# Optimization experiments

Hardware: AMD Instinct MI355X
Metric: run time of the kernel (lower is better)

The kernel has to match this reference:

```python
import jax, jax.numpy as jnp
import numpy as np

HEADS = 8
DIM_HEAD = 64
LN_EPS = 1e-5


def _layernorm(x, gamma, beta):
    mu = jnp.mean(x, axis=-1, keepdims=True)
    var = jnp.var(x, axis=-1, keepdims=True)
    return (x - mu) * jax.lax.rsqrt(var + LN_EPS) * gamma + beta


def setup_inputs() -> dict:
    key = jax.random.key(0)
    ks = jax.random.split(key, 5)
    B, N, D = 1, 16384, 512
    return {
        "x": jax.random.normal(ks[0], (B, N, D), dtype=jnp.float32),
        "ln_gamma": jnp.ones((D,), dtype=jnp.float32),
        "ln_beta": jnp.zeros((D,), dtype=jnp.float32),
        "w_qkv": jax.random.normal(ks[1], (D, 3 * D), dtype=jnp.float32) * (D ** -0.5),
        "agent": jax.random.normal(ks[2], (HEADS, 512, DIM_HEAD), dtype=jnp.float32) * (DIM_HEAD ** -0.5),
        "w_out": jax.random.normal(ks[3], (D, D), dtype=jnp.float32) * (D ** -0.5),
        "b_out": jnp.zeros((D,), dtype=jnp.float32),
    }


def reference(x, ln_gamma, ln_beta, w_qkv, agent, w_out, b_out):
    # TransLayer: x + Mask_Agent_Attention(LayerNorm(x))
    B, N, D = x.shape
    xn = _layernorm(x, ln_gamma, ln_beta)

    qkv = xn @ w_qkv                                   # [B, N, 3D]
    q, k, v = jnp.split(qkv, 3, axis=-1)
    # [B, H, N, d]
    q = q.reshape(B, N, HEADS, DIM_HEAD).transpose(0, 2, 1, 3)
    k = k.reshape(B, N, HEADS, DIM_HEAD).transpose(0, 2, 1, 3)
    v = v.reshape(B, N, HEADS, DIM_HEAD).transpose(0, 2, 1, 3)

    scale = DIM_HEAD ** -0.5  # tem=0 -> classical 1/sqrt(d) scaling

    # agents aggregate values: softmax over keys  [B, H, A, N]
    attn1 = jax.nn.softmax(jnp.einsum('had,bhnd->bhan', agent, k) * scale, axis=-1)
    agent_v = jnp.einsum('bhan,bhnd->bhad', attn1, v)  # [B, H, A, d]

    # queries attend to agents: softmax over agents  [B, H, N, A]
    attn2 = jax.nn.softmax(jnp.einsum('bhnd,had->bhna', q, agent) * scale, axis=-1)
    out = jnp.einsum('bhna,bhad->bhnd', attn2, agent_v)  # [B, H, N, d]

    out = out + v  # residual=True: value residual inside attention
    out = out.transpose(0, 2, 1, 3).reshape(B, N, D)
    out = out @ w_out + b_out
    return x + out
```

## Files before the change

kernel.cpp:

```cpp
#include <hip/hip_runtime.h>
#include <stdint.h>

typedef unsigned short u16;
typedef __attribute__((ext_vector_type(8))) short bf16x8;
typedef __attribute__((ext_vector_type(4))) float f32x4;

__device__ __forceinline__ float bf2f(u16 u){
  union { uint32_t i; float f; } v; v.i = ((uint32_t)u) << 16; return v.f;
}
__device__ __forceinline__ u16 f2bf(float f){
  union { float fl; uint32_t i; } v; v.fl = f;
  uint32_t r = v.i + 0x7FFFu + ((v.i >> 16) & 1u);
  return (u16)(r >> 16);
}
__device__ __forceinline__ uint32_t cvt_pk_bf16(float lo, float hi){
  uint32_t r;
  asm("v_cvt_pk_bf16_f32 %0, %1, %2" : "=v"(r) : "v"(lo), "v"(hi));
  return r;
}
__device__ __forceinline__ f32x4 mfma16(bf16x8 a, bf16x8 b, f32x4 c){
  return __builtin_amdgcn_mfma_f32_16x16x32_bf16(a, b, c, 0, 0, 0);
}
__device__ __forceinline__ void gload16(const u16* g, u16* l){
  __builtin_amdgcn_global_load_lds((const __attribute__((address_space(1))) void*)g,
                                   (__attribute__((address_space(3))) void*)l, 16, 0, 0);
}

__global__ __launch_bounds__(256) void k_conv_bf(const float* __restrict__ in, u16* __restrict__ out, int n, float scale){
  int i = (blockIdx.x * 256 + threadIdx.x) * 4;
  if (i >= n) return;
  float4 v = *(const float4*)(in + i);
  ushort4 o; o.x=f2bf(v.x*scale); o.y=f2bf(v.y*scale); o.z=f2bf(v.z*scale); o.w=f2bf(v.w*scale);
  *(ushort4*)(out + i) = o;
}

__global__ __launch_bounds__(256) void k_transp(const float* __restrict__ in, u16* __restrict__ out, int R, int C){
  __shared__ u16 tile[64][68];
  int c0 = blockIdx.x * 64, r0 = blockIdx.y * 64;
  int tr = threadIdx.x >> 4;
  int tc = (threadIdx.x & 15) * 4;
  for (int rr = 0; rr < 4; rr++){
    int r = rr * 16 + tr;
    float4 v = *(const float4*)(in + (size_t)(r0 + r) * C + c0 + tc);
    ushort4 o; o.x=f2bf(v.x); o.y=f2bf(v.y); o.z=f2bf(v.z); o.w=f2bf(v.w);
    *(ushort4*)&tile[r][tc] = o;
  }
  __syncthreads();
  for (int rr = 0; rr < 4; rr++){
    int oc = rr * 16 + tr;
    ushort4 o;
    o.x = tile[tc+0][oc]; o.y = tile[tc+1][oc]; o.z = tile[tc+2][oc]; o.w = tile[tc+3][oc];
    *(ushort4*)(out + (size_t)(c0 + oc) * R + r0 + tc) = o;
  }
}

__global__ __launch_bounds__(256) void k_transp_v(const u16* __restrict__ qkv, u16* __restrict__ vT){
  __shared__ u16 tile[64][68];
  int n0 = blockIdx.x * 64;
  int c0 = blockIdx.y * 64;
  int tr = threadIdx.x >> 4;
  int tc = (threadIdx.x & 15) * 4;
  for (int rr = 0; rr < 4; rr++){
    int r = rr * 16 + tr;
    ushort4 v = *(const ushort4*)(qkv + (size_t)(n0 + r) * 1536 + 1024 + c0 + tc);
    *(ushort4*)&tile[r][tc] = v;
  }
  __syncthreads();
  for (int rr = 0; rr < 4; rr++){
    int oc = rr * 16 + tr;
    ushort4 o;
    o.x = tile[tc+0][oc]; o.y = tile[tc+1][oc]; o.z = tile[tc+2][oc]; o.w = tile[tc+3][oc];
    *(ushort4*)(vT + (size_t)(c0 + oc) * 16384 + n0 + tc) = o;
  }
}

__global__ __launch_bounds__(128) void k_ln(const float* __restrict__ x, const float* __restrict__ g,
                                            const float* __restrict__ b, u16* __restrict__ xn){
  int row = blockIdx.x;
  int t = threadIdx.x;
  float4 v = *(const float4*)(x + (size_t)row * 512 + t * 4);
  float s = v.x + v.y + v.z + v.w;
  float q = v.x*v.x + v.y*v.y + v.z*v.z + v.w*v.w;
  for (int o = 32; o > 0; o >>= 1){ s += __shfl_down(s, o); q += __shfl_down(q, o); }
  __shared__ float red[4];
  if ((t & 63) == 0){ red[(t >> 6) * 2] = s; red[(t >> 6) * 2 + 1] = q; }
  __syncthreads();
  float mu  = (red[0] + red[2]) * (1.0f/512.0f);
  float var = (red[1] + red[3]) * (1.0f/512.0f) - mu * mu;
  float rs = rsqrtf(var + 1e-5f);
  float4 gv = *(const float4*)(g + t * 4);
  float4 bv = *(const float4*)(b + t * 4);
  ushort4 o;
  o.x = f2bf((v.x - mu) * rs * gv.x + bv.x);
  o.y = f2bf((v.y - mu) * rs * gv.y + bv.y);
  o.z = f2bf((v.z - mu) * rs * gv.z + bv.z);
  o.w = f2bf((v.w - mu) * rs * gv.w + bv.w);
  *(ushort4*)(xn + (size_t)row * 512 + t * 4) = o;
}

__global__ __launch_bounds__(256) void k_gemm_qkv(const u16* __restrict__ A, const u16* __restrict__ Bt,
                                                  u16* __restrict__ C){
  __shared__ u16 a_lds[128 * 64];
  __shared__ u16 b_lds[128 * 64];
  int m0 = blockIdx.x * 128, n0 = blockIdx.y * 128;
  int t = threadIdx.x, w = t >> 6, l = t & 63;
  int wm = (w >> 1) * 64, wn = (w & 1) * 64;
  int lr = l & 15, kb0 = (l >> 4) * 8;
  const u16* gA = A  + (size_t)(m0 + w*32 + (l >> 3)) * 512 + (l & 7) * 8;
  const u16* gB = Bt + (size_t)(n0 + w*32 + (l >> 3)) * 512 + (l & 7) * 8;
  u16* lA = &a_lds[(w*32) * 64];
  u16* lB = &b_lds[(w*32) * 64];
  f32x4 acc[4][4];
  for (int i=0;i<4;i++) for (int j=0;j<4;j++) acc[i][j] = {0.f,0.f,0.f,0.f};
  for (int k0 = 0; k0 < 512; k0 += 64){
    __syncthreads();
    #pragma unroll
    for (int i = 0; i < 4; i++){
      gload16(gA + k0 + (size_t)i*8*512, lA + i*8*64);
      gload16(gB + k0 + (size_t)i*8*512, lB + i*8*64);
    }
    __syncthreads();
    #pragma unroll
    for (int kk = 0; kk < 64; kk += 32){
      int kb = kb0 + kk;
      bf16x8 av[4], bv[4];
      for (int mt=0;mt<4;mt++) av[mt] = *(const bf16x8*)&a_lds[(wm + mt*16 + lr)*64 + kb];
      for (int nt=0;nt<4;nt++) bv[nt] = *(const bf16x8*)&b_lds[(wn + nt*16 + lr)*64 + kb];
      for (int mt=0;mt<4;mt++) for (int nt=0;nt<4;nt++)
        acc[mt][nt] = mfma16(av[mt], bv[nt], acc[mt][nt]);
    }
  }
  int rr = (l >> 4) * 4, cc = l & 15;
  for (int mt=0;mt<4;mt++) for (int nt=0;nt<4;nt++)
    for (int j=0;j<4;j++){
      int r = m0 + wm + mt*16 + rr + j;
      int c = n0 + wn + nt*16 + cc;
      C[(size_t)r * 1536 + c] = f2bf(acc[mt][nt][j]);
    }
}

__global__ __launch_bounds__(256) void k_gemm_out(const u16* __restrict__ A, const u16* __restrict__ Bt,
                                                  const float* __restrict__ x, const float* __restrict__ bias,
                                                  float* __restrict__ y){
  __shared__ u16 a_lds[128 * 64];
  __shared__ u16 b_lds[128 * 64];
  int m0 = blockIdx.x * 128, n0 = blockIdx.y * 128;
  int t = threadIdx.x, w = t >> 6, l = t & 63;
  int wm = (w >> 1) * 64, wn = (w & 1) * 64;
  int lr = l & 15, kb0 = (l >> 4) * 8;
  const u16* gA = A  + (size_t)(m0 + w*32 + (l >> 3)) * 512 + (l & 7) * 8;
  const u16* gB = Bt + (size_t)(n0 + w*32 + (l >> 3)) * 512 + (l & 7) * 8;
  u16* lA = &a_lds[(w*32) * 64];
  u16* lB = &b_lds[(w*32) * 64];
  f32x4 acc[4][4];
  for (int i=0;i<4;i++) for (int j=0;j<4;j++) acc[i][j] = {0.f,0.f,0.f,0.f};
  for (int k0 = 0; k0 < 512; k0 += 64){
    __syncthreads();
    #pragma unroll
    for (int i = 0; i < 4; i++){
      gload16(gA + k0 + (size_t)i*8*512, lA + i*8*64);
      gload16(gB + k0 + (size_t)i*8*512, lB + i*8*64);
    }
    __syncthreads();
    #pragma unroll
    for (int kk = 0; kk < 64; kk += 32){
      int kb = kb0 + kk;
      bf16x8 av[4], bv[4];
      for (int mt=0;mt<4;mt++) av[mt] = *(const bf16x8*)&a_lds[(wm + mt*16 + lr)*64 + kb];
      for (int nt=0;nt<4;nt++) bv[nt] = *(const bf16x8*)&b_lds[(wn + nt*16 + lr)*64 + kb];
      for (int mt=0;mt<4;mt++) for (int nt=0;nt<4;nt++)
        acc[mt][nt] = mfma16(av[mt], bv[nt], acc[mt][nt]);
    }
  }
  int rr = (l >> 4) * 4, cc = l & 15;
  for (int mt=0;mt<4;mt++) for (int nt=0;nt<4;nt++)
    for (int j=0;j<4;j++){
      int r = m0 + wm + mt*16 + rr + j;
      int c = n0 + wn + nt*16 + cc;
      y[(size_t)r * 512 + c] = acc[mt][nt][j] + bias[c] + x[(size_t)r * 512 + c];
    }
}

__global__ __launch_bounds__(256) void k_agent_agg(const u16* __restrict__ agbf, const u16* __restrict__ qkv,
                                                   const u16* __restrict__ vT,
                                                   float* __restrict__ nump, float* __restrict__ denp){
  int L = blockIdx.x;
  int g = (L >> 6) * 8 + (L & 7);
  int m = (L >> 3) & 7;
  int h = g >> 4, ch = g & 15, a0 = m * 64;

  __shared__ u16 ag[64][72];
  __shared__ u16 kt[64][72];
  __shared__ u16 vt[64][72];
  __shared__ u16 pt[64][72];
  int t = threadIdx.x, w = t >> 6, l = t & 63;

  for (int i = 0; i < 2; i++){
    int flat = t + 256 * i;
    int r = flat >> 3, c = (flat & 7) * 8;
    *(uint4*)&ag[r][c] = *(const uint4*)(agbf + (size_t)(h * 512 + a0 + r) * 64 + c);
  }

  bf16x8 ones;
  for (int i = 0; i < 8; i++) ones[i] = (short)0x3F80;

  f32x4 acc2[4];
  for (int i=0;i<4;i++) acc2[i] = {0.f,0.f,0.f,0.f};
  f32x4 accd = {0.f,0.f,0.f,0.f};

  for (int sub = 0; sub < 16; sub++){
    int n0 = ch * 1024 + sub * 64;
    __syncthreads();
    {
      int flat = t;
      int r = flat >> 3, c = (flat & 7) * 8;
      *(uint4*)&kt[r][c] = *(const uint4*)(qkv + (size_t)(n0 + r) * 1536 + 512 + h * 64 + c);
      int flat2 = t + 256;
      int r2 = flat2 >> 3, c2 = (flat2 & 7) * 8;
      *(uint4*)&kt[r2][c2] = *(const uint4*)(qkv + (size_t)(n0 + r2) * 1536 + 512 + h * 64 + c2);
      *(uint4*)&vt[r][c]   = *(const uint4*)(vT + ((size_t)(h * 64 + r) << 14) + n0 + c);
      *(uint4*)&vt[r2][c2] = *(const uint4*)(vT + ((size_t)(h * 64 + r2) << 14) + n0 + c2);
    }
    __syncthreads();

    f32x4 s[4];
    for (int nt=0;nt<4;nt++) s[nt] = {0.f,0.f,0.f,0.f};
    for (int kk = 0; kk < 64; kk += 32){
      int kb = kk + (l >> 4) * 8;
      bf16x8 kf = *(const bf16x8*)&kt[w*16 + (l & 15)][kb];
      for (int nt=0;nt<4;nt++){
        bf16x8 af = *(const bf16x8*)&ag[nt*16 + (l & 15)][kb];
        s[nt] = mfma16(kf, af, s[nt]);
      }
    }
    int nb = w*16 + (l >> 4) * 4;
    for (int nt=0;nt<4;nt++){
      int a = nt*16 + (l & 15);
      uint32_t w0 = cvt_pk_bf16(__builtin_amdgcn_exp2f(s[nt][0]), __builtin_amdgcn_exp2f(s[nt][1]));
      uint32_t w1 = cvt_pk_bf16(__builtin_amdgcn_exp2f(s[nt][2]), __builtin_amdgcn_exp2f(s[nt][3]));
      uint2 o; o.x = w0; o.y = w1;
      *(uint2*)&pt[a][nb] = o;
    }
    __syncthreads();

    for (int kk = 0; kk < 64; kk += 32){
      int kb = kk + (l >> 4) * 8;
      bf16x8 vf = *(const bf16x8*)&vt[w*16 + (l & 15)][kb];
      for (int mt=0;mt<4;mt++){
        bf16x8 pf = *(const bf16x8*)&pt[mt*16 + (l & 15)][kb];
        acc2[mt] = mfma16(pf, vf, acc2[mt]);
      }
      bf16x8 pw = *(const bf16x8*)&pt[w*16 + (l & 15)][kb];
      accd = mfma16(ones, pw, accd);
    }
  }

  size_t base = ((size_t)(h * 16 + ch) * 512 + a0) * 64;
  for (int mt=0;mt<4;mt++)
    #pragma unroll
    for (int j=0;j<4;j++){
      int a = mt*16 + (l>>4)*4 + j;
      int d = w*16 + (l&15);
      nump[base + (size_t)a*64 + d] = acc2[mt][j];
    }
  if (l < 16) denp[(size_t)(h*16 + ch) * 512 + a0 + w*16 + l] = accd[0];
}

__global__ __launch_bounds__(64) void k_agent_reduce(const float* __restrict__ nump, const float* __restrict__ denp,
                                                     u16* __restrict__ avtg){
  int h = blockIdx.x >> 9;
  int a = blockIdx.x & 511;
  int d = threadIdx.x;
  float num = 0.f, den = 0.f;
  for (int c = 0; c < 16; c++){
    num += nump[((size_t)(h * 16 + c) * 512 + a) * 64 + d];
    den += denp[(size_t)(h * 16 + c) * 512 + a];
  }
  avtg[((size_t)h * 64 + d) * 512 + a] = f2bf(num / den);
}

__global__ __launch_bounds__(256) void k_qattn(const u16* __restrict__ qkv, const u16* __restrict__ agbf,
                                               const u16* __restrict__ avtg, u16* __restrict__ atto){
  int n0 = blockIdx.x * 64;
  int h  = blockIdx.y;
  __shared__ u16 qt[64][72];
  __shared__ u16 ag[64][72];
  __shared__ u16 avt[64][72];
  __shared__ u16 pt[64][72];
  __shared__ float dnf[64];
  int t = threadIdx.x, w = t >> 6, l = t & 63;

  for (int i = 0; i < 2; i++){
    int flat = t + 256 * i;
    int r = flat >> 3, c = (flat & 7) * 8;
    *(uint4*)&qt[r][c] = *(const uint4*)(qkv + (size_t)(n0 + r) * 1536 + h * 64 + c);
  }

  bf16x8 ones;
  for (int i = 0; i < 8; i++) ones[i] = (short)0x3F80;

  f32x4 acc[4];
  for (int i=0;i<4;i++) acc[i] = {0.f,0.f,0.f,0.f};
  f32x4 accd = {0.f,0.f,0.f,0.f};

  for (int at = 0; at < 8; at++){
    int a0 = at * 64;
    __syncthreads();
    for (int i = 0; i < 2; i++){
      int flat = t + 256 * i;
      int r = flat >> 3, c = (flat & 7) * 8;
      *(uint4*)&ag[r][c]  = *(const uint4*)(agbf + (size_t)(h * 512 + a0 + r) * 64 + c);
      *(uint4*)&avt[r][c] = *(const uint4*)(avtg + (size_t)(h * 64 + r) * 512 + a0 + c);
    }
    __syncthreads();

    f32x4 s[4];
    for (int nt=0;nt<4;nt++) s[nt] = {0.f,0.f,0.f,0.f};
    for (int kk = 0; kk < 64; kk += 32){
      int kb = kk + (l >> 4) * 8;
      bf16x8 af = *(const bf16x8*)&ag[w*16 + (l & 15)][kb];
      for (int nt=0;nt<4;nt++){
        bf16x8 qf = *(const bf16x8*)&qt[nt*16 + (l & 15)][kb];
        s[nt] = mfma16(af, qf, s[nt]);
      }
    }
    int ab = w*16 + (l >> 4) * 4;
    for (int nt=0;nt<4;nt++){
      int n = nt*16 + (l & 15);
      uint32_t w0 = cvt_pk_bf16(__builtin_amdgcn_exp2f(s[nt][0]), __builtin_amdgcn_exp2f(s[nt][1]));
      uint32_t w1 = cvt_pk_bf16(__builtin_amdgcn_exp2f(s[nt][2]), __builtin_amdgcn_exp2f(s[nt][3]));
      uint2 o; o.x = w0; o.y = w1;
      *(uint2*)&pt[n][ab] = o;
    }
    __syncthreads();

    for (int kk = 0; kk < 64; kk += 32){
      int kb = kk + (l >> 4) * 8;
      bf16x8 vf = *(const bf16x8*)&avt[w*16 + (l & 15)][kb];
      for (int mt=0;mt<4;mt++){
        bf16x8 pf = *(const bf16x8*)&pt[mt*16 + (l & 15)][kb];
        acc[mt] = mfma16(pf, vf, acc[mt]);
      }
      bf16x8 pw = *(const bf16x8*)&pt[w*16 + (l & 15)][kb];
      accd = mfma16(ones, pw, accd);
    }
  }

  if (l < 16) dnf[w*16 + l] = accd[0];
  __syncthreads();
  if (t < 64) dnf[t] = __builtin_amdgcn_rcpf(dnf[t]);
  __syncthreads();

  int d = w*16 + (l & 15);
  for (int mt=0;mt<4;mt++){
    #pragma unroll
    for (int j=0;j<4;j++){
      int n = mt*16 + (l>>4)*4 + j;
      float v = bf2f(qkv[(size_t)(n0 + n) * 1536 + 1024 + h * 64 + d]);
      atto[(size_t)(n0 + n) * 512 + h * 64 + d] = f2bf(acc[mt][j] * dnf[n] + v);
    }
  }
}

extern "C" void kernel_launch(void* const* d_in, const int* in_sizes, int n_in,
                              void* d_out, int out_size, void* d_ws, size_t ws_size,
                              hipStream_t stream) {
  const float* x     = (const float*)d_in[0];
  const float* gamma = (const float*)d_in[1];
  const float* beta  = (const float*)d_in[2];
  const float* w_qkv = (const float*)d_in[3];
  const float* agent = (const float*)d_in[4];
  const float* w_out = (const float*)d_in[5];
  const float* b_out = (const float*)d_in[6];
  float* y = (float*)d_out;

  char* ws = (char*)d_ws;
  u16*   xn    = (u16*)  (ws + 0);
  u16*   vT    = (u16*)  (ws + 0);
  u16*   qkv   = (u16*)  (ws + 16777216);
  u16*   wqkvt = (u16*)  (ws + 67108864);
  u16*   woutt = (u16*)  (ws + 68681728);
  u16*   agbf  = (u16*)  (ws + 69206016);
  u16*   avtg  = (u16*)  (ws + 69730304);
  u16*   atto  = (u16*)  (ws + 70254592);
  float* nump  = (float*)(ws + 87031808);
  float* denp  = (float*)(ws + 103809024);

  k_conv_bf   <<<dim3(256),     dim3(256), 0, stream>>>(agent, agbf, 8*512*64, 0.125f * 1.44269504089f);
  k_transp    <<<dim3(24, 8),   dim3(256), 0, stream>>>(w_qkv, wqkvt, 512, 1536);
  k_transp    <<<dim3(8, 8),    dim3(256), 0, stream>>>(w_out, woutt, 512, 512);
  k_ln        <<<dim3(16384),   dim3(128), 0, stream>>>(x, gamma, beta, xn);
  k_gemm_qkv  <<<dim3(128, 12), dim3(256), 0, stream>>>(xn, wqkvt, qkv);
  k_transp_v  <<<dim3(256, 8),  dim3(256), 0, stream>>>(qkv, vT);
  k_agent_agg <<<dim3(1024),    dim3(256), 0, stream>>>(agbf, qkv, vT, nump, denp);
  k_agent_reduce<<<dim3(4096),  dim3(64),  0, stream>>>(nump, denp, avtg);
  k_qattn     <<<dim3(256, 8),  dim3(256), 0, stream>>>(qkv, agbf, avtg, atto);
  k_gemm_out  <<<dim3(128, 4),  dim3(256), 0, stream>>>(atto, woutt, x, b_out, y);
}
```

Measured before the change: 176.4 us.

## Double-buffer LDS tiles in QKV and output GEMMs to overlap loads with MFMA

Both projection GEMMs now keep two LDS buffers for A and B tiles and issue the global-to-LDS loads for the next K-step before computing on the current one. This replaces the old pattern of two barriers per K-step with load-then-compute serialization, so memory latency is meant to hide behind MFMA work. It doubles LDS use per block to 64 KB, which may reduce occupancy. The K loop is also fully unrolled.

```diff
diff --git a/kernel.cpp b/kernel.cpp
--- a/kernel.cpp
+++ b/kernel.cpp
@@ -100,36 +100,54 @@
 
 __global__ __launch_bounds__(256) void k_gemm_qkv(const u16* __restrict__ A, const u16* __restrict__ Bt,
                                                   u16* __restrict__ C){
-  __shared__ u16 a_lds[128 * 64];
-  __shared__ u16 b_lds[128 * 64];
+  __shared__ u16 aL[2][128 * 64];
+  __shared__ u16 bL[2][128 * 64];
   int m0 = blockIdx.x * 128, n0 = blockIdx.y * 128;
   int t = threadIdx.x, w = t >> 6, l = t & 63;
   int wm = (w >> 1) * 64, wn = (w & 1) * 64;
   int lr = l & 15, kb0 = (l >> 4) * 8;
   const u16* gA = A  + (size_t)(m0 + w*32 + (l >> 3)) * 512 + (l & 7) * 8;
   const u16* gB = Bt + (size_t)(n0 + w*32 + (l >> 3)) * 512 + (l & 7) * 8;
-  u16* lA = &a_lds[(w*32) * 64];
-  u16* lB = &b_lds[(w*32) * 64];
+  int ldsOff = (w*32) * 64;
   f32x4 acc[4][4];
   for (int i=0;i<4;i++) for (int j=0;j<4;j++) acc[i][j] = {0.f,0.f,0.f,0.f};
-  for (int k0 = 0; k0 < 512; k0 += 64){
-    __syncthreads();
+
+  auto stage = [&](int buf, int k0){
     #pragma unroll
     for (int i = 0; i < 4; i++){
-      gload16(gA + k0 + (size_t)i*8*512, lA + i*8*64);
-      gload16(gB + k0 + (size_t)i*8*512, lB + i*8*64);
-    }
-    __syncthreads();
+      gload16(gA + k0 + (size_t)i*8*512, &aL[buf][ldsOff + i*8*64]);
+      gload16(gB + k0 + (size_t)i*8*512, &bL[buf][ldsOff + i*8*64]);
+    }
+  };
+  auto comp = [&](const u16* ab, const u16* bb){
     #pragma unroll
     for (int kk = 0; kk < 64; kk += 32){
       int kb = kb0 + kk;
       bf16x8 av[4], bv[4];
-      for (int mt=0;mt<4;mt++) av[mt] = *(const bf16x8*)&a_lds[(wm + mt*16 + lr)*64 + kb];
-      for (int nt=0;nt<4;nt++) bv[nt] = *(const bf16x8*)&b_lds[(wn + nt*16 + lr)*64 + kb];
-      for (int mt=0;mt<4;mt++) for (int nt=0;nt<4;nt++)
-        acc[mt][nt] = mfma16(av[mt], bv[nt], acc[mt][nt]);
-    }
-  }
+      #pragma unroll
+      for (int mt=0;mt<4;mt++) av[mt] = *(const bf16x8*)&ab[(wm + mt*16 + lr)*64 + kb];
+      #pragma unroll
+      for (int nt=0;nt<4;nt++) bv[nt] = *(const bf16x8*)&bb[(wn + nt*16 + lr)*64 + kb];
+      #pragma unroll
+      for (int mt=0;mt<4;mt++)
+        #pragma unroll
+        for (int nt=0;nt<4;nt++)
+          acc[mt][nt] = mfma16(av[mt], bv[nt], acc[mt][nt]);
+    }
+  };
+
+  stage(0, 0);
+  __syncthreads();
+  #pragma unroll
+  for (int tk = 0; tk < 8; tk += 2){
+    stage(1, (tk + 1) * 64);
+    comp(&aL[0][0], &bL[0][0]);
+    __syncthreads();
+    if (tk + 2 < 8) stage(0, (tk + 2) * 64);
+    comp(&aL[1][0], &bL[1][0]);
+    __syncthreads();
+  }
+
   int rr = (l >> 4) * 4, cc = l & 15;
   for (int mt=0;mt<4;mt++) for (int nt=0;nt<4;nt++)
     for (int j=0;j<4;j++){
@@ -142,36 +160,54 @@
 __global__ __launch_bounds__(256) void k_gemm_out(const u16* __restrict__ A, const u16* __restrict__ Bt,
                                                   const float* __restrict__ x, const float* __restrict__ bias,
                                                   float* __restrict__ y){
-  __shared__ u16 a_lds[128 * 64];
-  __shared__ u16 b_lds[128 * 64];
+  __shared__ u16 aL[2][128 * 64];
+  __shared__ u16 bL[2][128 * 64];
   int m0 = blockIdx.x * 128, n0 = blockIdx.y * 128;
   int t = threadIdx.x, w = t >> 6, l = t & 63;
   int wm = (w >> 1) * 64, wn = (w & 1) * 64;
   int lr = l & 15, kb0 = (l >> 4) * 8;
   const u16* gA = A  + (size_t)(m0 + w*32 + (l >> 3)) * 512 + (l & 7) * 8;
   const u16* gB = Bt + (size_t)(n0 + w*32 + (l >> 3)) * 512 + (l & 7) * 8;
-  u16* lA = &a_lds[(w*32) * 64];
-  u16* lB = &b_lds[(w*32) * 64];
+  int ldsOff = (w*32) * 64;
   f32x4 acc[4][4];
   for (int i=0;i<4;i++) for (int j=0;j<4;j++) acc[i][j] = {0.f,0.f,0.f,0.f};
-  for (int k0 = 0; k0 < 512; k0 += 64){
-    __syncthreads();
+
+  auto stage = [&](int buf, int k0){
     #pragma unroll
     for (int i = 0; i < 4; i++){
-      gload16(gA + k0 + (size_t)i*8*512, lA + i*8*64);
-      gload16(gB + k0 + (size_t)i*8*512, lB + i*8*64);
-    }
-    __syncthreads();
+      gload16(gA + k0 + (size_t)i*8*512, &aL[buf][ldsOff + i*8*64]);
+      gload16(gB + k0 + (size_t)i*8*512, &bL[buf][ldsOff + i*8*64]);
+    }
+  };
+  auto comp = [&](const u16* ab, const u16* bb){
     #pragma unroll
     for (int kk = 0; kk < 64; kk += 32){
       int kb = kb0 + kk;
       bf16x8 av[4], bv[4];
-      for (int mt=0;mt<4;mt++) av[mt] = *(const bf16x8*)&a_lds[(wm + mt*16 + lr)*64 + kb];
-      for (int nt=0;nt<4;nt++) bv[nt] = *(const bf16x8*)&b_lds[(wn + nt*16 + lr)*64 + kb];
-      for (int mt=0;mt<4;mt++) for (int nt=0;nt<4;nt++)
-        acc[mt][nt] = mfma16(av[mt], bv[nt], acc[mt][nt]);
-    }
-  }
+      #pragma unroll
+      for (int mt=0;mt<4;mt++) av[mt] = *(const bf16x8*)&ab[(wm + mt*16 + lr)*64 + kb];
+      #pragma unroll
+      for (int nt=0;nt<4;nt++) bv[nt] = *(const bf16x8*)&bb[(wn + nt*16 + lr)*64 + kb];
+      #pragma unroll
+      for (int mt=0;mt<4;mt++)
+        #pragma unroll
+        for (int nt=0;nt<4;nt++)
+          acc[mt][nt] = mfma16(av[mt], bv[nt], acc[mt][nt]);
+    }
+  };
+
+  stage(0, 0);
+  __syncthreads();
+  #pragma unroll
+  for (int tk = 0; tk < 8; tk += 2){
+    stage(1, (tk + 1) * 64);
+    comp(&aL[0][0], &bL[0][0]);
+    __syncthreads();
+    if (tk + 2 < 8) stage(0, (tk + 2) * 64);
+    comp(&aL[1][0], &bL[1][0]);
+    __syncthreads();
+  }
+
   int rr = (l >> 4) * 4, cc = l & 15;
   for (int mt=0;mt<4;mt++) for (int nt=0;nt<4;nt++)
     for (int j=0;j<4;j++){
```

Result: slower. 182.1 us (+3.3%).
